# Optimization experiments

Measured on AMD Instinct MI355X. Metric: run time of the kernel, lower is better.

## Reference

```python
import jax, jax.numpy as jnp
import numpy as np

N_NODES = 50000
N_EDGES = 800000
D_IN = 128
D_HID = 128
D_OUT = 128


def setup_inputs() -> dict:
    key = jax.random.key(0)
    ks = jax.random.split(key, 12)
    features = jax.random.normal(ks[0], (N_NODES, D_IN), dtype=jnp.float32)
    src = jax.random.randint(ks[1], (N_EDGES,), 0, N_NODES, dtype=jnp.int32)
    dst = jax.random.randint(ks[2], (N_EDGES,), 0, N_NODES, dtype=jnp.int32)
    s_in = 1.0 / np.sqrt(D_IN)
    s_hid = 1.0 / np.sqrt(D_HID)
    W1 = jax.random.normal(ks[3], (D_IN, D_HID), dtype=jnp.float32) * s_in
    b1 = jnp.zeros((D_HID,), dtype=jnp.float32)
    W2 = jax.random.normal(ks[4], (D_HID, D_HID), dtype=jnp.float32) * s_hid
    b2 = jnp.zeros((D_HID,), dtype=jnp.float32)
    W3 = jax.random.normal(ks[5], (D_HID, D_OUT), dtype=jnp.float32) * s_hid
    b3 = jnp.zeros((D_OUT,), dtype=jnp.float32)
    policy_w = jax.random.normal(ks[6], (D_OUT, 1), dtype=jnp.float32) * s_hid
    policy_b = jnp.zeros((1,), dtype=jnp.float32)
    value_w = jax.random.normal(ks[7], (D_OUT, 1), dtype=jnp.float32) * s_hid
    value_b = jnp.zeros((1,), dtype=jnp.float32)
    return {
        "features": features, "src": src, "dst": dst,
        "W1": W1, "b1": b1, "W2": W2, "b2": b2, "W3": W3, "b3": b3,
        "policy_w": policy_w, "policy_b": policy_b,
        "value_w": value_w, "value_b": value_b,
    }


def _graph_conv(h, src, dst, deg_inv, W, b, act):
    # DGL GraphConv with norm='left': scale source features by 1/out_degree,
    # sum messages over incoming edges, then linear transform + bias (+ act).
    hn = h * deg_inv  # [N, d]
    agg = jax.ops.segment_sum(hn[src], dst, num_segments=N_NODES)  # SpMM: [N, d]
    out = agg @ W + b
    return jax.nn.relu(out) if act else out


def reference(features, src, dst, W1, b1, W2, b2, W3, b3,
              policy_w, policy_b, value_w, value_b):
    ones = jnp.ones((src.shape[0],), dtype=features.dtype)
    deg = jax.ops.segment_sum(ones, src, num_segments=N_NODES)  # out-degree
    deg_inv = (1.0 / jnp.clip(deg, 1.0))[:, None]  # [N, 1]

    h = _graph_conv(features, src, dst, deg_inv, W1, b1, act=True)
    h = _graph_conv(h, src, dst, deg_inv, W2, b2, act=True)
    h = _graph_conv(h, src, dst, deg_inv, W3, b3, act=False)  # last layer: no activation

    mN = jnp.mean(h, axis=0, keepdims=True)  # mean readout over nodes, [1, D_OUT]
    PI = h @ policy_w + policy_b  # [N, 1]
    V = mN @ value_w + value_b    # [1, 1]
    return PI, V
```

## Files before the change

kernel.cpp:

```cpp
#include <hip/hip_runtime.h>


#define N_NODES 50000
#define N_EDGES 800000
#define D 128
#define NSH 8
#define PROWS (N_NODES + 8)
#define PANEL ((size_t)PROWS * 16)
#define NC 64
#define CSZ (N_EDGES / NC)
#define NW (N_NODES / 2)
#define CS_CAP (N_EDGES + 8 * N_NODES)


__global__ __launch_bounds__(512) void k_hist3(const int* __restrict__ src, const int* __restrict__ dst,
                                               unsigned* __restrict__ ghd16, unsigned* __restrict__ ghs16) {
    __shared__ unsigned h[NW];
    const int arr = blockIdx.x & 1;
    const int c   = blockIdx.x >> 1;
    const int t = threadIdx.x;
    for (int i = t; i < NW; i += 512) h[i] = 0u;
    __syncthreads();
    const int* __restrict__ col = arr ? src : dst;
    const int e0 = c * CSZ, e1 = e0 + CSZ;
    for (int e = e0 + t; e < e1; e += 512) {
        int n = col[e];
        atomicAdd(&h[n >> 1], 1u << ((n & 1) << 4));
    }
    __syncthreads();
    unsigned* __restrict__ outp = (arr ? ghs16 : ghd16) + (size_t)c * NW;
    for (int i = t; i < NW; i += 512) outp[i] = h[i];
}

__global__ __launch_bounds__(256) void k_merge3(unsigned* __restrict__ ghd16, const unsigned* __restrict__ ghs16,
                                                int* __restrict__ rowcnt, int* __restrict__ rowtrue,
                                                float* __restrict__ dinv) {
    int w = blockIdx.x * 256 + threadIdx.x;
    if (w >= NW) return;
    unsigned runlo = 0, runhi = 0;
#pragma unroll
    for (int c = 0; c < NC; c++) {
        unsigned v = ghd16[(size_t)c * NW + w];
        ghd16[(size_t)c * NW + w] = runlo | (runhi << 16);
        runlo += v & 0xffffu; runhi += v >> 16;
    }
    rowtrue[2 * w]     = (int)runlo;
    rowtrue[2 * w + 1] = (int)runhi;
    rowcnt[2 * w]      = (int)((runlo + 7u) & ~7u);
    rowcnt[2 * w + 1]  = (int)((runhi + 7u) & ~7u);
    unsigned dlo = 0, dhi = 0;
#pragma unroll
    for (int c = 0; c < NC; c++) {
        unsigned v = ghs16[(size_t)c * NW + w];
        dlo += v & 0xffffu; dhi += v >> 16;
    }
    dinv[2 * w]     = 1.0f / (float)(dlo > 1u ? dlo : 1u);
    dinv[2 * w + 1] = 1.0f / (float)(dhi > 1u ? dhi : 1u);
}

__global__ __launch_bounds__(1024) void k_scan1(const int* __restrict__ cnt, int* __restrict__ excl,
                                                int* __restrict__ blocksum, int n) {
    __shared__ int wsum[16];
    int i = blockIdx.x * 1024 + threadIdx.x;
    int v = (i < n) ? cnt[i] : 0;
    int lane = threadIdx.x & 63, wid = threadIdx.x >> 6;
    int x = v;
#pragma unroll
    for (int off = 1; off < 64; off <<= 1) {
        int y = __shfl_up(x, off, 64);
        if (lane >= off) x += y;
    }
    if (lane == 63) wsum[wid] = x;
    __syncthreads();
    if (threadIdx.x == 0) {
        int run = 0;
        for (int w = 0; w < 16; w++) { int t = wsum[w]; wsum[w] = run; run += t; }
        blocksum[blockIdx.x] = run;
    }
    __syncthreads();
    if (i < n) excl[i] = (x - v) + wsum[wid];
}

__global__ void k_scan2(const int* __restrict__ blocksum, int* __restrict__ blockoff,
                        int* __restrict__ rowptr_last, int nblk) {
    if (threadIdx.x == 0) {
        int run = 0;
        for (int b = 0; b < nblk; b++) { int t = blocksum[b]; blockoff[b] = run; run += t; }
        rowptr_last[0] = run;
    }
}

__global__ __launch_bounds__(1024) void k_scan3(int* __restrict__ excl, const int* __restrict__ blockoff, int n) {
    int i = blockIdx.x * 1024 + threadIdx.x;
    if (i < n) excl[i] += blockoff[blockIdx.x];
}

__global__ __launch_bounds__(512) void k_fill3(const int* __restrict__ src, const int* __restrict__ dst,
                                               const int* __restrict__ rowptr, const unsigned* __restrict__ ghd16,
                                               unsigned short* __restrict__ cs16) {
    __shared__ unsigned cnt[NW];
    const int c = blockIdx.x;
    const int t = threadIdx.x;
    for (int i = t; i < NW; i += 512) cnt[i] = 0u;
    __syncthreads();
    const unsigned* __restrict__ basep = ghd16 + (size_t)c * NW;
    const int e0 = c * CSZ, e1 = e0 + CSZ;
    for (int e = e0 + t; e < e1; e += 512) {
        int d = dst[e];
        int sh = (d & 1) << 4;
        unsigned old = atomicAdd(&cnt[d >> 1], 1u << sh);
        int p = (int)((old >> sh) & 0xffffu);
        int base = (int)((basep[d >> 1] >> sh) & 0xffffu);
        cs16[rowptr[d] + base + p] = (unsigned short)src[e];
    }
}

__global__ __launch_bounds__(256) void k_pad(const int* __restrict__ rowptr, const int* __restrict__ rowtrue,
                                             unsigned short* __restrict__ cs16,
                                             float* __restrict__ bufA, float* __restrict__ bufB) {
    int n = blockIdx.x * 256 + threadIdx.x;
    if (n < N_NODES) {
        int e0 = rowptr[n] + rowtrue[n], e1 = rowptr[n + 1];
        for (int e = e0; e < e1; e++) cs16[e] = (unsigned short)N_NODES;
    }
    if (blockIdx.x == 0) {
        int t = threadIdx.x;
        float* b = (t & 128) ? bufB : bufA;
        int p = (t >> 4) & 7, cc = t & 15;
        b[(size_t)p * PANEL + (size_t)N_NODES * 16 + cc] = 0.f;
    }
}


__global__ __launch_bounds__(256) void k_panelize(const float* __restrict__ in, const float* __restrict__ dinv,
                                                  float* __restrict__ outp) {
    int tid = blockIdx.x * 256 + threadIdx.x;
    if (tid >= N_NODES * 32) return;
    int p = tid / (N_NODES * 4);
    int r = tid - p * (N_NODES * 4);
    int node = r >> 2, qq = r & 3;
    float w = dinv[node];
    float4 v = *reinterpret_cast<const float4*>(&in[(size_t)node * D + p * 16 + qq * 4]);
    v.x *= w; v.y *= w; v.z *= w; v.w *= w;
    *reinterpret_cast<float4*>(&outp[(size_t)p * PANEL + (size_t)node * 16 + qq * 4]) = v;
}


__global__ __launch_bounds__(256) void k_agg(const float* __restrict__ hp,
                                             const int* __restrict__ rp, const unsigned short* __restrict__ cs16,
                                             float* __restrict__ outp) {
    const int l4 = threadIdx.x & 3;
    const int grp = threadIdx.x >> 2;
    const int slice = blockIdx.x & (NSH - 1);
    const int node = (blockIdx.x >> 3) * 64 + grp;
    if (node >= N_NODES) return;
    const float* __restrict__ pan = hp + (size_t)slice * PANEL + l4 * 4;
    int s0 = rp[node], s1 = rp[node + 1];
    float4 acc = {0.f, 0.f, 0.f, 0.f};
    for (int e = s0; e < s1; e += 8) {
        int4 r = *reinterpret_cast<const int4*>(&cs16[e]);
        int i0 = r.x & 0xffff, i1 = (r.x >> 16) & 0xffff;
        int i2 = r.y & 0xffff, i3 = (r.y >> 16) & 0xffff;
        int i4 = r.z & 0xffff, i5 = (r.z >> 16) & 0xffff;
        int i6 = r.w & 0xffff, i7 = (r.w >> 16) & 0xffff;
        float4 a0 = *reinterpret_cast<const float4*>(&pan[(size_t)i0 * 16]);
        float4 a1 = *reinterpret_cast<const float4*>(&pan[(size_t)i1 * 16]);
        float4 a2 = *reinterpret_cast<const float4*>(&pan[(size_t)i2 * 16]);
        float4 a3 = *reinterpret_cast<const float4*>(&pan[(size_t)i3 * 16]);
        float4 a4 = *reinterpret_cast<const float4*>(&pan[(size_t)i4 * 16]);
        float4 a5 = *reinterpret_cast<const float4*>(&pan[(size_t)i5 * 16]);
        float4 a6 = *reinterpret_cast<const float4*>(&pan[(size_t)i6 * 16]);
        float4 a7 = *reinterpret_cast<const float4*>(&pan[(size_t)i7 * 16]);
        acc.x += ((a0.x + a1.x) + (a2.x + a3.x)) + ((a4.x + a5.x) + (a6.x + a7.x));
        acc.y += ((a0.y + a1.y) + (a2.y + a3.y)) + ((a4.y + a5.y) + (a6.y + a7.y));
        acc.z += ((a0.z + a1.z) + (a2.z + a3.z)) + ((a4.z + a5.z) + (a6.z + a7.z));
        acc.w += ((a0.w + a1.w) + (a2.w + a3.w)) + ((a4.w + a5.w) + (a6.w + a7.w));
    }
    *reinterpret_cast<float4*>(&outp[(size_t)slice * PANEL + (size_t)node * 16 + l4 * 4]) = acc;
}


__global__ __launch_bounds__(256) void k_gemm(const float* __restrict__ in, const float* __restrict__ W,
                                              const float* __restrict__ bias, float* __restrict__ out,
                                              int nrows, int relu,
                                              const float* __restrict__ dscale,
                                              const float* __restrict__ pw, const float* __restrict__ pb,
                                              float* __restrict__ pi_out, float* __restrict__ colsum) {
    __shared__ float wl[D * D];
    __shared__ float at[D * 32];
    int t = threadIdx.x;
    const int head = (pw != nullptr);
    for (int i = t; i < D * D / 4; i += 256)
        reinterpret_cast<float4*>(wl)[i] = reinterpret_cast<const float4*>(W)[i];
    const int tx = t & 31;
    const int ty = t >> 5;
    const int ldrow = t & 31;
    const int ldc   = t >> 5;
    float4 bv = reinterpret_cast<const float4*>(bias)[tx];
    float4 pwv = head ? reinterpret_cast<const float4*>(pw)[tx] : float4{0.f, 0.f, 0.f, 0.f};
    float pb0 = head ? pb[0] : 0.f;
    const int op = tx >> 2, oq = tx & 3;
    float cs0 = 0.f, cs1 = 0.f, cs2 = 0.f, cs3 = 0.f;
    int ntiles = (nrows + 31) / 32;

    for (int tile = blockIdx.x; tile < ntiles; tile += gridDim.x) {
        int row0 = tile * 32;
        __syncthreads();
        {
            int gr = row0 + ldrow;
            float va[16];
            if (gr < nrows) {
                const float4* ap = reinterpret_cast<const float4*>(&in[(size_t)ldc * PANEL + (size_t)gr * 16]);
#pragma unroll
                for (int qq = 0; qq < 4; qq++) {
                    float4 v = ap[qq];
                    va[qq * 4 + 0] = v.x; va[qq * 4 + 1] = v.y;
                    va[qq * 4 + 2] = v.z; va[qq * 4 + 3] = v.w;
                }
            } else {
#pragma unroll
                for (int qq = 0; qq < 16; qq++) va[qq] = 0.f;
            }
            int kb = ldc * 16;
#pragma unroll
            for (int j = 0; j < 16; j++) at[(kb + j) * 32 + ldrow] = va[j];
        }
        __syncthreads();

        float acc[4][4];
#pragma unroll
        for (int j = 0; j < 4; j++)
#pragma unroll
            for (int c = 0; c < 4; c++) acc[j][c] = 0.f;

#pragma unroll 8
        for (int k = 0; k < D; k++) {
            float4 a = *reinterpret_cast<const float4*>(&at[k * 32 + ty * 4]);
            float4 w = *reinterpret_cast<const float4*>(&wl[k * D + tx * 4]);
            acc[0][0] += a.x * w.x; acc[0][1] += a.x * w.y; acc[0][2] += a.x * w.z; acc[0][3] += a.x * w.w;
            acc[1][0] += a.y * w.x; acc[1][1] += a.y * w.y; acc[1][2] += a.y * w.z; acc[1][3] += a.y * w.w;
            acc[2][0] += a.z * w.x; acc[2][1] += a.z * w.y; acc[2][2] += a.z * w.z; acc[2][3] += a.z * w.w;
            acc[3][0] += a.w * w.x; acc[3][1] += a.w * w.y; acc[3][2] += a.w * w.z; acc[3][3] += a.w * w.w;
        }

#pragma unroll
        for (int j = 0; j < 4; j++) {
            int gr = row0 + ty * 4 + j;
            if (gr < nrows) {
                float4 o;
                o.x = acc[j][0] + bv.x; o.y = acc[j][1] + bv.y;
                o.z = acc[j][2] + bv.z; o.w = acc[j][3] + bv.w;
                if (relu) {
                    o.x = fmaxf(o.x, 0.f); o.y = fmaxf(o.y, 0.f);
                    o.z = fmaxf(o.z, 0.f); o.w = fmaxf(o.w, 0.f);
                }
                if (head) {
                    cs0 += o.x; cs1 += o.y; cs2 += o.z; cs3 += o.w;
                    float pr = o.x * pwv.x + o.y * pwv.y + o.z * pwv.z + o.w * pwv.w;
#pragma unroll
                    for (int off = 16; off > 0; off >>= 1) pr += __shfl_xor(pr, off, 32);
                    if (tx == 0) pi_out[gr] = pr + pb0;
                } else {
                    if (dscale) {
                        float w = dscale[gr];
                        o.x *= w; o.y *= w; o.z *= w; o.w *= w;
                    }
                    *reinterpret_cast<float4*>(&out[(size_t)op * PANEL + (size_t)gr * 16 + oq * 4]) = o;
                }
            }
        }
    }

    if (head) {
        __syncthreads();
        float* csl = at;
        if (t < D) csl[t] = 0.f;
        __syncthreads();
        atomicAdd(&csl[tx * 4 + 0], cs0);
        atomicAdd(&csl[tx * 4 + 1], cs1);
        atomicAdd(&csl[tx * 4 + 2], cs2);
        atomicAdd(&csl[tx * 4 + 3], cs3);
        __syncthreads();
        if (t < D) atomicAdd(&colsum[t], csl[t]);
    }
}


__global__ __launch_bounds__(128) void k_value(const float* __restrict__ colsum, const float* __restrict__ vw,
                                               const float* __restrict__ vb, float* __restrict__ out) {
    __shared__ float red[128];
    int t = threadIdx.x;
    red[t] = (colsum[t] * (1.0f / (float)N_NODES)) * vw[t];
    __syncthreads();
    for (int s = 64; s > 0; s >>= 1) {
        if (t < s) red[t] += red[t + s];
        __syncthreads();
    }
    if (t == 0) out[0] = red[0] + vb[0];
}

__global__ __launch_bounds__(64) void k_ws_too_small(float* __restrict__ out, int n) {
    int i = blockIdx.x * 64 + threadIdx.x;
    if (i < n) out[i] = -1e30f;
}


extern "C" void kernel_launch(void* const* d_in, const int* in_sizes, int n_in,
                              void* d_out, int out_size, void* d_ws, size_t ws_size,
                              hipStream_t stream) {
    const float* features = (const float*)d_in[0];
    const int*   src      = (const int*)d_in[1];
    const int*   dst      = (const int*)d_in[2];
    const float* W1 = (const float*)d_in[3];
    const float* b1 = (const float*)d_in[4];
    const float* W2 = (const float*)d_in[5];
    const float* b2 = (const float*)d_in[6];
    const float* W3 = (const float*)d_in[7];
    const float* b3 = (const float*)d_in[8];
    const float* pw = (const float*)d_in[9];
    const float* pb = (const float*)d_in[10];
    const float* vw = (const float*)d_in[11];
    const float* vb = (const float*)d_in[12];
    float* out = (float*)d_out;

    char* ws = (char*)d_ws;
    size_t off = 0;
    auto alloc = [&](size_t bytes) -> char* {
        char* p = ws + off;
        off += (bytes + 255) & ~(size_t)255;
        return p;
    };
    float* dinv     = (float*)alloc((size_t)N_NODES * 4);
    int*   rowptr   = (int*)alloc((size_t)(N_NODES + 1) * 4);
    int*   rowcnt   = (int*)alloc((size_t)N_NODES * 4);
    int*   rowtrue  = (int*)alloc((size_t)N_NODES * 4);
    int*   blocksum = (int*)alloc(64 * 4);
    int*   blockoff = (int*)alloc(64 * 4);
    float* colsum   = (float*)alloc(D * 4);
    unsigned short* cs16 = (unsigned short*)alloc((size_t)CS_CAP * 2);
    float* bufA     = (float*)alloc((size_t)NSH * PANEL * 4);
    float* bufB     = (float*)alloc((size_t)NSH * PANEL * 4);

    unsigned* ghd16 = (unsigned*)bufB;
    unsigned* ghs16 = ghd16 + (size_t)NC * NW;

    if (off > ws_size) {
        k_ws_too_small<<<(out_size + 63) / 64, 64, 0, stream>>>(out, out_size);
        return;
    }

    hipMemsetAsync(colsum, 0, (size_t)D * 4, stream);

    k_hist3<<<2 * NC, 512, 0, stream>>>(src, dst, ghd16, ghs16);
    k_merge3<<<(NW + 255) / 256, 256, 0, stream>>>(ghd16, ghs16, rowcnt, rowtrue, dinv);

    int nblk = (N_NODES + 1023) / 1024;
    k_scan1<<<nblk, 1024, 0, stream>>>(rowcnt, rowptr, blocksum, N_NODES);
    k_scan2<<<1, 64, 0, stream>>>(blocksum, blockoff, rowptr + N_NODES, nblk);
    k_scan3<<<nblk, 1024, 0, stream>>>(rowptr, blockoff, N_NODES);
    k_fill3<<<NC, 512, 0, stream>>>(src, dst, rowptr, ghd16, cs16);
    k_pad<<<(N_NODES + 255) / 256, 256, 0, stream>>>(rowptr, rowtrue, cs16, bufA, bufB);

    k_panelize<<<(N_NODES * 32 + 255) / 256, 256, 0, stream>>>(features, dinv, bufA);

    int aggblocks = ((N_NODES + 63) / 64) * NSH;
    k_agg<<<aggblocks, 256, 0, stream>>>(bufA, rowptr, cs16, bufB);
    k_gemm<<<512, 256, 0, stream>>>(bufB, W1, b1, bufB, N_NODES, 1, dinv,
                                    nullptr, nullptr, nullptr, nullptr);
    k_agg<<<aggblocks, 256, 0, stream>>>(bufB, rowptr, cs16, bufA);
    k_gemm<<<512, 256, 0, stream>>>(bufA, W2, b2, bufA, N_NODES, 1, dinv,
                                    nullptr, nullptr, nullptr, nullptr);
    k_agg<<<aggblocks, 256, 0, stream>>>(bufA, rowptr, cs16, bufB);
    k_gemm<<<512, 256, 0, stream>>>(bufB, W3, b3, nullptr, N_NODES, 0, nullptr,
                                    pw, pb, out, colsum);

    k_value<<<1, 128, 0, stream>>>(colsum, vw, vb, out + N_NODES);
}
```

Measured before the change: 309.7 us.

## Enlarge GEMM tile to 64 rows with 4x8 micro-tiles and prefetched A halves

Reworks the dense transform kernel so each block handles 64 rows per tile, with each thread computing a 4x8 output micro-tile instead of 4x4. The K dimension is split into two 64-wide halves staged through shared memory, and the next tile's first half is loaded into registers while the current tile computes. The aim is to raise arithmetic intensity per shared-memory read and hide global latency. In exchange it uses more registers per thread, which can lower occupancy, and adds extra barriers per tile.

```diff
diff --git a/kernel.cpp b/kernel.cpp
--- a/kernel.cpp
+++ b/kernel.cpp
@@ -187,85 +187,120 @@
                                               const float* __restrict__ pw, const float* __restrict__ pb,
                                               float* __restrict__ pi_out, float* __restrict__ colsum) {
     __shared__ float wl[D * D];
-    __shared__ float at[D * 32];
+    __shared__ float at[64 * 64];
     int t = threadIdx.x;
     const int head = (pw != nullptr);
     for (int i = t; i < D * D / 4; i += 256)
         reinterpret_cast<float4*>(wl)[i] = reinterpret_cast<const float4*>(W)[i];
-    const int tx = t & 31;
-    const int ty = t >> 5;
-    const int ldrow = t & 31;
-    const int ldc   = t >> 5;
-    float4 bv = reinterpret_cast<const float4*>(bias)[tx];
-    float4 pwv = head ? reinterpret_cast<const float4*>(pw)[tx] : float4{0.f, 0.f, 0.f, 0.f};
+    const int tx = t & 15;
+    const int ro = t >> 4;
+    const int sr = t & 63;
+    const int sq = t >> 6;
+    float4 bv1 = reinterpret_cast<const float4*>(bias)[tx];
+    float4 bv2 = reinterpret_cast<const float4*>(bias)[16 + tx];
+    float4 pw1 = head ? reinterpret_cast<const float4*>(pw)[tx]      : float4{0, 0, 0, 0};
+    float4 pw2 = head ? reinterpret_cast<const float4*>(pw)[16 + tx] : float4{0, 0, 0, 0};
     float pb0 = head ? pb[0] : 0.f;
-    const int op = tx >> 2, oq = tx & 3;
-    float cs0 = 0.f, cs1 = 0.f, cs2 = 0.f, cs3 = 0.f;
-    int ntiles = (nrows + 31) / 32;
-
-    for (int tile = blockIdx.x; tile < ntiles; tile += gridDim.x) {
-        int row0 = tile * 32;
-        __syncthreads();
+    float4 cs1 = {0, 0, 0, 0}, cs2 = {0, 0, 0, 0};
+    int ntiles = (nrows + 63) / 64;
+
+#define LOADA(va, r0, h)                                                              \
+    {                                                                                 \
+        int gr_ = (r0) + sr;                                                          \
+        if (gr_ < nrows) {                                                            \
+            const float4* ap_ = reinterpret_cast<const float4*>(                      \
+                &in[(size_t)((h) * 4 + sq) * PANEL + (size_t)gr_ * 16]);              \
+            va[0] = ap_[0]; va[1] = ap_[1]; va[2] = ap_[2]; va[3] = ap_[3];           \
+        } else {                                                                      \
+            va[0] = va[1] = va[2] = va[3] = float4{0, 0, 0, 0};                       \
+        }                                                                             \
+    }
+
+#define WRITEA(va)                                                                    \
+    _Pragma("unroll")                                                                 \
+    for (int q = 0; q < 4; q++) {                                                     \
+        int kk_ = sq * 16 + q * 4;                                                    \
+        at[(kk_ + 0) * 64 + sr] = va[q].x; at[(kk_ + 1) * 64 + sr] = va[q].y;         \
+        at[(kk_ + 2) * 64 + sr] = va[q].z; at[(kk_ + 3) * 64 + sr] = va[q].w;         \
+    }
+
+#define KLOOP(H)                                                                      \
+    {                                                                                 \
+        const float* __restrict__ wlh = wl + (H) * 64 * D;                            \
+        _Pragma("unroll 8")                                                           \
+        for (int kk = 0; kk < 64; kk++) {                                             \
+            float4 a  = *reinterpret_cast<const float4*>(&at[kk * 64 + ro * 4]);      \
+            float4 w1 = *reinterpret_cast<const float4*>(&wlh[kk * D + tx * 4]);      \
+            float4 w2 = *reinterpret_cast<const float4*>(&wlh[kk * D + 64 + tx * 4]); \
+            acc[0][0] += a.x * w1.x; acc[0][1] += a.x * w1.y; acc[0][2] += a.x * w1.z; acc[0][3] += a.x * w1.w; \
+            acc[0][4] += a.x * w2.x; acc[0][5] += a.x * w2.y; acc[0][6] += a.x * w2.z; acc[0][7] += a.x * w2.w; \
+            acc[1][0] += a.y * w1.x; acc[1][1] += a.y * w1.y; acc[1][2] += a.y * w1.z; acc[1][3] += a.y * w1.w; \
+            acc[1][4] += a.y * w2.x; acc[1][5] += a.y * w2.y; acc[1][6] += a.y * w2.z; acc[1][7] += a.y * w2.w; \
+            acc[2][0] += a.z * w1.x; acc[2][1] += a.z * w1.y; acc[2][2] += a.z * w1.z; acc[2][3] += a.z * w1.w; \
+            acc[2][4] += a.z * w2.x; acc[2][5] += a.z * w2.y; acc[2][6] += a.z * w2.z; acc[2][7] += a.z * w2.w; \
+            acc[3][0] += a.w * w1.x; acc[3][1] += a.w * w1.y; acc[3][2] += a.w * w1.z; acc[3][3] += a.w * w1.w; \
+            acc[3][4] += a.w * w2.x; acc[3][5] += a.w * w2.y; acc[3][6] += a.w * w2.z; acc[3][7] += a.w * w2.w; \
+        }                                                                             \
+    }
+
+    float4 vaA[4], vaB[4];
+    int tile0 = blockIdx.x;
+    if (tile0 < ntiles) LOADA(vaA, tile0 * 64, 0);
+
+    for (int tile = tile0; tile < ntiles; tile += gridDim.x) {
+        int row0 = tile * 64;
+        float acc[4][8];
+#pragma unroll
+        for (int j = 0; j < 4; j++)
+#pragma unroll
+            for (int c = 0; c < 8; c++) acc[j][c] = 0.f;
+
+        __syncthreads();
+        WRITEA(vaA);
+        LOADA(vaB, row0, 1);
+        __syncthreads();
+        KLOOP(0);
+        __syncthreads();
+        WRITEA(vaB);
         {
-            int gr = row0 + ldrow;
-            float va[16];
+            int nt = tile + gridDim.x;
+            if (nt < ntiles) LOADA(vaA, nt * 64, 0);
+        }
+        __syncthreads();
+        KLOOP(1);
+
+#pragma unroll
+        for (int j = 0; j < 4; j++) {
+            int gr = row0 + ro * 4 + j;
             if (gr < nrows) {
-                const float4* ap = reinterpret_cast<const float4*>(&in[(size_t)ldc * PANEL + (size_t)gr * 16]);
-#pragma unroll
-                for (int qq = 0; qq < 4; qq++) {
-                    float4 v = ap[qq];
-                    va[qq * 4 + 0] = v.x; va[qq * 4 + 1] = v.y;
-                    va[qq * 4 + 2] = v.z; va[qq * 4 + 3] = v.w;
-                }
-            } else {
-#pragma unroll
-                for (int qq = 0; qq < 16; qq++) va[qq] = 0.f;
-            }
-            int kb = ldc * 16;
-#pragma unroll
-            for (int j = 0; j < 16; j++) at[(kb + j) * 32 + ldrow] = va[j];
-        }
-        __syncthreads();
-
-        float acc[4][4];
-#pragma unroll
-        for (int j = 0; j < 4; j++)
-#pragma unroll
-            for (int c = 0; c < 4; c++) acc[j][c] = 0.f;
-
-#pragma unroll 8
-        for (int k = 0; k < D; k++) {
-            float4 a = *reinterpret_cast<const float4*>(&at[k * 32 + ty * 4]);
-            float4 w = *reinterpret_cast<const float4*>(&wl[k * D + tx * 4]);
-            acc[0][0] += a.x * w.x; acc[0][1] += a.x * w.y; acc[0][2] += a.x * w.z; acc[0][3] += a.x * w.w;
-            acc[1][0] += a.y * w.x; acc[1][1] += a.y * w.y; acc[1][2] += a.y * w.z; acc[1][3] += a.y * w.w;
-            acc[2][0] += a.z * w.x; acc[2][1] += a.z * w.y; acc[2][2] += a.z * w.z; acc[2][3] += a.z * w.w;
-            acc[3][0] += a.w * w.x; acc[3][1] += a.w * w.y; acc[3][2] += a.w * w.z; acc[3][3] += a.w * w.w;
-        }
-
-#pragma unroll
-        for (int j = 0; j < 4; j++) {
-            int gr = row0 + ty * 4 + j;
-            if (gr < nrows) {
-                float4 o;
-                o.x = acc[j][0] + bv.x; o.y = acc[j][1] + bv.y;
-                o.z = acc[j][2] + bv.z; o.w = acc[j][3] + bv.w;
+                float4 o1, o2;
+                o1.x = acc[j][0] + bv1.x; o1.y = acc[j][1] + bv1.y;
+                o1.z = acc[j][2] + bv1.z; o1.w = acc[j][3] + bv1.w;
+                o2.x = acc[j][4] + bv2.x; o2.y = acc[j][5] + bv2.y;
+                o2.z = acc[j][6] + bv2.z; o2.w = acc[j][7] + bv2.w;
                 if (relu) {
-                    o.x = fmaxf(o.x, 0.f); o.y = fmaxf(o.y, 0.f);
-                    o.z = fmaxf(o.z, 0.f); o.w = fmaxf(o.w, 0.f);
+                    o1.x = fmaxf(o1.x, 0.f); o1.y = fmaxf(o1.y, 0.f);
+                    o1.z = fmaxf(o1.z, 0.f); o1.w = fmaxf(o1.w, 0.f);
+                    o2.x = fmaxf(o2.x, 0.f); o2.y = fmaxf(o2.y, 0.f);
+                    o2.z = fmaxf(o2.z, 0.f); o2.w = fmaxf(o2.w, 0.f);
                 }
                 if (head) {
-                    cs0 += o.x; cs1 += o.y; cs2 += o.z; cs3 += o.w;
-                    float pr = o.x * pwv.x + o.y * pwv.y + o.z * pwv.z + o.w * pwv.w;
-#pragma unroll
-                    for (int off = 16; off > 0; off >>= 1) pr += __shfl_xor(pr, off, 32);
+                    cs1.x += o1.x; cs1.y += o1.y; cs1.z += o1.z; cs1.w += o1.w;
+                    cs2.x += o2.x; cs2.y += o2.y; cs2.z += o2.z; cs2.w += o2.w;
+                    float pr = o1.x * pw1.x + o1.y * pw1.y + o1.z * pw1.z + o1.w * pw1.w
+                             + o2.x * pw2.x + o2.y * pw2.y + o2.z * pw2.z + o2.w * pw2.w;
+#pragma unroll
+                    for (int m = 8; m > 0; m >>= 1) pr += __shfl_xor(pr, m, 16);
                     if (tx == 0) pi_out[gr] = pr + pb0;
                 } else {
                     if (dscale) {
                         float w = dscale[gr];
-                        o.x *= w; o.y *= w; o.z *= w; o.w *= w;
+                        o1.x *= w; o1.y *= w; o1.z *= w; o1.w *= w;
+                        o2.x *= w; o2.y *= w; o2.z *= w; o2.w *= w;
                     }
-                    *reinterpret_cast<float4*>(&out[(size_t)op * PANEL + (size_t)gr * 16 + oq * 4]) = o;
+                    size_t base1 = (size_t)(tx >> 2) * PANEL + (size_t)gr * 16 + (tx & 3) * 4;
+                    *reinterpret_cast<float4*>(&out[base1]) = o1;
+                    *reinterpret_cast<float4*>(&out[base1 + 4 * PANEL]) = o2;
                 }
             }
         }
@@ -276,13 +311,20 @@
         float* csl = at;
         if (t < D) csl[t] = 0.f;
         __syncthreads();
-        atomicAdd(&csl[tx * 4 + 0], cs0);
-        atomicAdd(&csl[tx * 4 + 1], cs1);
-        atomicAdd(&csl[tx * 4 + 2], cs2);
-        atomicAdd(&csl[tx * 4 + 3], cs3);
+        atomicAdd(&csl[tx * 4 + 0], cs1.x);
+        atomicAdd(&csl[tx * 4 + 1], cs1.y);
+        atomicAdd(&csl[tx * 4 + 2], cs1.z);
+        atomicAdd(&csl[tx * 4 + 3], cs1.w);
+        atomicAdd(&csl[64 + tx * 4 + 0], cs2.x);
+        atomicAdd(&csl[64 + tx * 4 + 1], cs2.y);
+        atomicAdd(&csl[64 + tx * 4 + 2], cs2.z);
+        atomicAdd(&csl[64 + tx * 4 + 3], cs2.w);
         __syncthreads();
         if (t < D) atomicAdd(&colsum[t], csl[t]);
     }
+#undef LOADA
+#undef WRITEA
+#undef KLOOP
 }
 
 
```

After: 321.6 us. 3.8% more time.
